# Performance work log

Measured on AMD Instinct MI355X. Metric: run time of the kernel, lower is better.

Reference implementation:

```python
import jax, jax.numpy as jnp
import numpy as np
import math

PHI = (1 + math.sqrt(5)) / 2
ALPHA = 1 / PHI          # residual scale
BETA = 1 / PHI ** 2      # sparse-matmul scale
DIM = 1910
NZ = int(DIM * DIM / PHI)


def setup_inputs() -> dict:
    key = jax.random.key(0)
    kx, ki, kv = jax.random.split(key, 3)
    x = jax.random.normal(kx, (8, 4096, DIM), dtype=jnp.float32)
    W_indices = jax.random.randint(ki, (2, NZ), 0, DIM, dtype=jnp.int32)
    W_values = jax.random.normal(kv, (NZ,), dtype=jnp.float32) / math.sqrt(DIM)
    return {"x": x, "W_indices": W_indices, "W_values": W_values}


def reference(x, W_indices, W_values):
    dim = x.shape[-1]
    # COO -> dense: duplicate (row,col) entries sum, matching torch.sparse semantics.
    W = jnp.zeros((dim, dim), dtype=x.dtype).at[W_indices[0], W_indices[1]].add(W_values)
    orig_shape = x.shape
    xf = x.reshape(-1, dim)          # [tokens, dim]
    Wx = xf @ W.T                    # (W @ x.T).T == x @ W.T
    out = ALPHA * xf + BETA * Wx
    return out.reshape(orig_shape)
```

## Files before the change

kernel.cpp:

```cpp
#include <hip/hip_runtime.h>
#include <hip/hip_bf16.h>
#include <stdint.h>

#define DIMV 1910
#define KP   1920
#define NT   30
#define TT   120
#define PHI_F  1.6180339887498949f
#define BETA_F 0.3819660112501051f

typedef __attribute__((ext_vector_type(4))) float f32x4;
typedef __attribute__((ext_vector_type(8))) short bf16x8;
typedef __attribute__((ext_vector_type(8))) unsigned short u16x8;

__device__ __forceinline__ void gl16(const void* g, void* l) {
    __builtin_amdgcn_global_load_lds(
        (const __attribute__((address_space(1))) void*)(uintptr_t)g,
        (__attribute__((address_space(3))) void*)(uint32_t)(uintptr_t)l,
        16, 0, 0);
}

__global__ void k_prep(const float* __restrict__ x, unsigned short* __restrict__ xb, int total8,
                       const int* __restrict__ ridx, const int* __restrict__ cidx,
                       const float* __restrict__ vals, float* __restrict__ Wd, int nz) {
    const int tid  = threadIdx.x;
    const int half = (int)gridDim.x >> 1;
    const int b    = (int)blockIdx.x >> 1;
    const int stride = half * 256;
    if ((blockIdx.x & 1) == 0) {
        for (int i = b * 256 + tid; i < total8; i += stride) {
            int v = i * 8;
            int row = v / KP;
            int col = v - row * KP;
            u16x8 o;
            if (col + 8 <= DIMV) {
                const float2* s = (const float2*)(x + (size_t)row * DIMV + col);
                float2 f0 = s[0], f1 = s[1], f2 = s[2], f3 = s[3];
                float f[8] = {f0.x, f0.y, f1.x, f1.y, f2.x, f2.y, f3.x, f3.y};
#pragma unroll
                for (int j = 0; j < 8; ++j) {
                    __hip_bfloat16 bb = __float2bfloat16(f[j]);
                    o[j] = *reinterpret_cast<unsigned short*>(&bb);
                }
            } else {
#pragma unroll
                for (int j = 0; j < 8; ++j) {
                    int c = col + j;
                    float fv = (c < DIMV) ? x[(size_t)row * DIMV + c] : 0.f;
                    __hip_bfloat16 bb = __float2bfloat16(fv);
                    o[j] = *reinterpret_cast<unsigned short*>(&bb);
                }
            }
            *(u16x8*)(xb + (size_t)v) = o;
        }
    } else {
        for (int i = b * 256 + tid; i < nz; i += stride)
            atomicAdd(Wd + (size_t)ridx[i] * DIMV + cidx[i], vals[i]);
    }
}

__global__ void k_build_w(const float* __restrict__ Wd, unsigned short* __restrict__ Wb, int total8) {
    int stride = gridDim.x * blockDim.x;
    for (int i = blockIdx.x * blockDim.x + threadIdx.x; i < total8; i += stride) {
        int v = i * 8;
        int n = v / KP;
        int k = v - n * KP;
        u16x8 o;
#pragma unroll
        for (int j = 0; j < 8; ++j) {
            int kk = k + j;
            float fv = (n < DIMV && kk < DIMV) ? Wd[(size_t)n * DIMV + kk] : 0.f;
            if (kk == n && n < DIMV) fv += PHI_F;
            __hip_bfloat16 b = __float2bfloat16(fv);
            o[j] = *reinterpret_cast<unsigned short*>(&b);
        }
        *(u16x8*)(Wb + (size_t)v) = o;
    }
}

__global__ __launch_bounds__(512, 2) void k_gemm(const short* __restrict__ A,
                                                 const short* __restrict__ B,
                                                 float* __restrict__ C) {
    __shared__ char lds[163840];

    const int bid = blockIdx.x;
    const int bmg = bid & 31;
    const int bn  = bid >> 5;

    const int tid = threadIdx.x;
    const int w   = tid >> 6;
    const int l   = tid & 63;
    const int wm  = w >> 2;
    const int wn  = w & 3;
    const int fr  = l & 15;
    const int q   = l >> 4;

    const int    srow = tid >> 3;
    const size_t KPB  = (size_t)KP * 2;
    const int    swz  = ((tid & 7) ^ (srow & 7)) * 16;
    const char*  bSrc = (const char*)B + (size_t)(bn * 256 + srow) * KPB + swz;
    const size_t sweep = (size_t)64 * KPB;
    char* stDst = lds + tid * 16;

    const int co0  = ((q    ) ^ (fr & 7)) * 16;
    const int co1  = ((4 + q) ^ (fr & 7)) * 16;
    const int aOff = (wm * 128 + fr) * 128;
    const int bOff = (wn * 64 + fr) * 128;

    f32x4 acc[8][4] = {};

#define STAGE_A(src, kk_, dstoff, s) gl16((src) + (size_t)(s) * sweep + (size_t)(kk_) * 128, stDst + (dstoff) + (s) * 8192)
#define STAGE_B(kk_, dstoff, s)      gl16(bSrc  + (size_t)(s) * sweep + (size_t)(kk_) * 128, stDst + 98304 + (dstoff) + (s) * 8192)

    const char* aSrc0 = (const char*)A + (size_t)(bmg * 256 + srow) * KPB + swz;
    const size_t mstep = (size_t)8192 * KPB;

#pragma unroll
    for (int s = 0; s < 4; ++s) STAGE_A(aSrc0, 0, 0, s);
#pragma unroll
    for (int s = 0; s < 4; ++s) STAGE_B(0, 0, s);
#pragma unroll
    for (int s = 0; s < 4; ++s) STAGE_A(aSrc0, 1, 32768, s);
    asm volatile("s_waitcnt vmcnt(4)" ::: "memory");
    __builtin_amdgcn_s_barrier();
    asm volatile("" ::: "memory");

    int boA = 0, stA = 65536;
    int boB = 0, stB = 32768;
    int tkR = 0;
    int kb1 = 1;
    int ka2 = 2;
    int mtR = 0;
    const char* aStage = aSrc0;

    for (int t = 0; t < TT; ++t) {
        const char* pa = lds + boA + aOff;
        const char* pb = lds + 98304 + boB + bOff;
        const bool stb = (t + 1 < TT);
        const bool sta = (t + 2 < TT);
        bf16x8 a[4][2], b0[2][2], b1[2][2];

#pragma unroll
        for (int mi = 0; mi < 4; ++mi) {
            a[mi][0] = *(const bf16x8*)(pa + mi * 2048 + co0);
            a[mi][1] = *(const bf16x8*)(pa + mi * 2048 + co1);
        }
#pragma unroll
        for (int ni = 0; ni < 2; ++ni) {
            b0[ni][0] = *(const bf16x8*)(pb + ni * 2048 + co0);
            b0[ni][1] = *(const bf16x8*)(pb + ni * 2048 + co1);
        }
        if (stb) { STAGE_B(kb1, stB, 0); STAGE_B(kb1, stB, 1); }
        asm volatile("s_waitcnt lgkmcnt(8)" ::: "memory");
        __builtin_amdgcn_s_barrier();
        asm volatile("s_waitcnt lgkmcnt(0)" ::: "memory");
        __builtin_amdgcn_sched_barrier(0);
        __builtin_amdgcn_s_setprio(1);
#pragma unroll
        for (int kk = 0; kk < 2; ++kk)
#pragma unroll
            for (int mi = 0; mi < 4; ++mi)
#pragma unroll
                for (int ni = 0; ni < 2; ++ni)
                    acc[mi][ni] = __builtin_amdgcn_mfma_f32_16x16x32_bf16(a[mi][kk], b0[ni][kk], acc[mi][ni], 0, 0, 0);
        __builtin_amdgcn_s_setprio(0);
        asm volatile("" ::: "memory");
        __builtin_amdgcn_s_barrier();
        asm volatile("" ::: "memory");

#pragma unroll
        for (int ni = 0; ni < 2; ++ni) {
            b1[ni][0] = *(const bf16x8*)(pb + 4096 + ni * 2048 + co0);
            b1[ni][1] = *(const bf16x8*)(pb + 4096 + ni * 2048 + co1);
        }
        if (stb) { STAGE_B(kb1, stB, 2); STAGE_B(kb1, stB, 3); }
        if (sta) { STAGE_A(aStage, ka2, stA, 0); STAGE_A(aStage, ka2, stA, 1); }
        asm volatile("" ::: "memory");
        __builtin_amdgcn_s_barrier();
        asm volatile("s_waitcnt lgkmcnt(0)" ::: "memory");
        __builtin_amdgcn_sched_barrier(0);
        __builtin_amdgcn_s_setprio(1);
#pragma unroll
        for (int kk = 0; kk < 2; ++kk)
#pragma unroll
            for (int mi = 0; mi < 4; ++mi)
#pragma unroll
                for (int ni = 0; ni < 2; ++ni)
                    acc[mi][ni + 2] = __builtin_amdgcn_mfma_f32_16x16x32_bf16(a[mi][kk], b1[ni][kk], acc[mi][ni + 2], 0, 0, 0);
        __builtin_amdgcn_s_setprio(0);
        asm volatile("" ::: "memory");
        __builtin_amdgcn_s_barrier();
        asm volatile("" ::: "memory");

#pragma unroll
        for (int mi = 0; mi < 4; ++mi) {
            a[mi][0] = *(const bf16x8*)(pa + 8192 + mi * 2048 + co0);
            a[mi][1] = *(const bf16x8*)(pa + 8192 + mi * 2048 + co1);
        }
        if (sta) { STAGE_A(aStage, ka2, stA, 2); STAGE_A(aStage, ka2, stA, 3); }
        asm volatile("" ::: "memory");
        __builtin_amdgcn_s_barrier();
        asm volatile("s_waitcnt lgkmcnt(0)" ::: "memory");
        __builtin_amdgcn_sched_barrier(0);
        __builtin_amdgcn_s_setprio(1);
#pragma unroll
        for (int kk = 0; kk < 2; ++kk)
#pragma unroll
            for (int mi = 0; mi < 4; ++mi)
#pragma unroll
                for (int ni = 0; ni < 2; ++ni)
                    acc[mi + 4][ni + 2] = __builtin_amdgcn_mfma_f32_16x16x32_bf16(a[mi][kk], b1[ni][kk], acc[mi + 4][ni + 2], 0, 0, 0);
#pragma unroll
        for (int kk = 0; kk < 2; ++kk)
#pragma unroll
            for (int mi = 0; mi < 4; ++mi)
#pragma unroll
                for (int ni = 0; ni < 2; ++ni)
                    acc[mi + 4][ni] = __builtin_amdgcn_mfma_f32_16x16x32_bf16(a[mi][kk], b0[ni][kk], acc[mi + 4][ni], 0, 0, 0);
        __builtin_amdgcn_s_setprio(0);
        if (sta) { asm volatile("s_waitcnt vmcnt(4)" ::: "memory"); }
        else     { asm volatile("s_waitcnt vmcnt(0)" ::: "memory"); }
        __builtin_amdgcn_s_barrier();
        asm volatile("" ::: "memory");

        if (tkR == NT - 1) {
            const int bm    = mtR * 32 + bmg;
            const int grow0 = bm * 256 + wm * 128 + q * 4;
            const int gcol0 = bn * 256 + wn * 64 + fr;
#pragma unroll
            for (int ei = 0; ei < 8; ++ei) {
#pragma unroll
                for (int ni = 0; ni < 4; ++ni) {
                    int gcol = gcol0 + ni * 16;
                    if (gcol < DIMV) {
                        size_t base = (size_t)(grow0 + ei * 16) * DIMV + gcol;
#pragma unroll
                        for (int r = 0; r < 4; ++r)
                            C[base + (size_t)r * DIMV] = BETA_F * acc[ei][ni][r];
                    }
                }
            }
            if (t + 1 < TT) {
#pragma unroll
                for (int ei = 0; ei < 8; ++ei)
#pragma unroll
                    for (int ni = 0; ni < 4; ++ni)
                        acc[ei][ni] = (f32x4)(0.f);
            }
            tkR = 0; ++mtR;
        } else ++tkR;

        boA = (boA == 65536) ? 0 : boA + 32768;
        stA = (stA == 65536) ? 0 : stA + 32768;
        boB ^= 32768;
        stB ^= 32768;
        if (++kb1 == NT) kb1 = 0;
        if (++ka2 == NT) { ka2 = 0; aStage += mstep; }
    }
#undef STAGE_A
#undef STAGE_B
}

extern "C" void kernel_launch(void* const* d_in, const int* in_sizes, int n_in,
                              void* d_out, int out_size, void* d_ws, size_t ws_size,
                              hipStream_t stream) {
    const float* x    = (const float*)d_in[0];
    const int*   widx = (const int*)d_in[1];
    const float* wval = (const float*)d_in[2];
    float* out = (float*)d_out;

    const int nz = in_sizes[2];
    const int M  = in_sizes[0] / DIMV;

    const size_t xb_bytes = (size_t)M * KP * 2;
    const size_t wb_bytes = (size_t)2048 * KP * 2;
    const size_t wd_bytes = (size_t)DIMV * DIMV * 4;
    char* ws = (char*)d_ws;
    unsigned short* xb = (unsigned short*)ws;
    unsigned short* Wb = (unsigned short*)(ws + xb_bytes);
    float*          Wd = (float*)(ws + xb_bytes + wb_bytes);
    if (ws_size < xb_bytes + wb_bytes + wd_bytes) return;

    hipMemsetAsync(Wd, 0, wd_bytes, stream);
    k_prep<<<2048, 256, 0, stream>>>(x, xb, M * KP / 8, widx, widx + nz, wval, Wd, nz);
    k_build_w<<<1800, 256, 0, stream>>>(Wd, Wb, KP * KP / 8);
    k_gemm<<<256, 512, 0, stream>>>((const short*)xb, (const short*)Wb, out);
}
```

Before: 390.2 us.

## Restructure GEMM main loop into two-phase double-buffered LDS with register prefetch

Replaces the four-phase loop (triple-buffered A, double-buffered B) with a two-phase loop. A and B are both double-buffered in LDS, which shrinks the shared allocation to 128 KB. Each iteration loads the next k-slice's first fragments into registers while the current second-half MMAs run, and issues all global→LDS stages for iteration t+2 in one group. This halves the barriers per iteration and lengthens the MFMA runs, at the cost of more live operand registers and a full vmcnt(0) wait each iteration.

```diff
diff --git a/kernel.cpp b/kernel.cpp
--- a/kernel.cpp
+++ b/kernel.cpp
@@ -81,7 +81,7 @@
 __global__ __launch_bounds__(512, 2) void k_gemm(const short* __restrict__ A,
                                                  const short* __restrict__ B,
                                                  float* __restrict__ C) {
-    __shared__ char lds[163840];
+    __shared__ char lds[131072];
 
     const int bid = blockIdx.x;
     const int bmg = bid & 31;
@@ -108,9 +108,16 @@
     const int bOff = (wn * 64 + fr) * 128;
 
     f32x4 acc[8][4] = {};
-
-#define STAGE_A(src, kk_, dstoff, s) gl16((src) + (size_t)(s) * sweep + (size_t)(kk_) * 128, stDst + (dstoff) + (s) * 8192)
-#define STAGE_B(kk_, dstoff, s)      gl16(bSrc  + (size_t)(s) * sweep + (size_t)(kk_) * 128, stDst + 98304 + (dstoff) + (s) * 8192)
+    bf16x8 aP0[8], aP1[8], bR0[4], bR1[4];
+
+#define STAGE_A(src, kk_, slot, s) gl16((src) + (size_t)(s) * sweep + (size_t)(kk_) * 128, stDst + (slot) + (s) * 8192)
+#define STAGE_B(kk_, slot, s)      gl16(bSrc  + (size_t)(s) * sweep + (size_t)(kk_) * 128, stDst + 65536 + (slot) + (s) * 8192)
+#define MM(bank, bb)                                                             \
+    _Pragma("unroll")                                                            \
+    for (int mi = 0; mi < 8; ++mi)                                               \
+        _Pragma("unroll")                                                        \
+        for (int ni = 0; ni < 4; ++ni)                                           \
+            acc[mi][ni] = __builtin_amdgcn_mfma_f32_16x16x32_bf16((bank)[mi], (bb)[ni], acc[mi][ni], 0, 0, 0);
 
     const char* aSrc0 = (const char*)A + (size_t)(bmg * 256 + srow) * KPB + swz;
     const size_t mstep = (size_t)8192 * KPB;
@@ -121,107 +128,65 @@
     for (int s = 0; s < 4; ++s) STAGE_B(0, 0, s);
 #pragma unroll
     for (int s = 0; s < 4; ++s) STAGE_A(aSrc0, 1, 32768, s);
-    asm volatile("s_waitcnt vmcnt(4)" ::: "memory");
+#pragma unroll
+    for (int s = 0; s < 4; ++s) STAGE_B(1, 32768, s);
+    asm volatile("s_waitcnt vmcnt(8)" ::: "memory");
     __builtin_amdgcn_s_barrier();
-    asm volatile("" ::: "memory");
-
-    int boA = 0, stA = 65536;
-    int boB = 0, stB = 32768;
-    int tkR = 0;
-    int kb1 = 1;
-    int ka2 = 2;
-    int mtR = 0;
+    __builtin_amdgcn_sched_barrier(0);
+#pragma unroll
+    for (int mi = 0; mi < 8; ++mi) aP0[mi] = *(const bf16x8*)(lds + aOff + mi * 2048 + co0);
+#pragma unroll
+    for (int ni = 0; ni < 4; ++ni) bR0[ni] = *(const bf16x8*)(lds + 65536 + bOff + ni * 2048 + co0);
+
+    int bo  = 0;
+    int k2  = 2;
+    int tkR = 0, mtR = 0;
     const char* aStage = aSrc0;
 
     for (int t = 0; t < TT; ++t) {
-        const char* pa = lds + boA + aOff;
-        const char* pb = lds + 98304 + boB + bOff;
-        const bool stb = (t + 1 < TT);
-        const bool sta = (t + 2 < TT);
-        bf16x8 a[4][2], b0[2][2], b1[2][2];
-
-#pragma unroll
-        for (int mi = 0; mi < 4; ++mi) {
-            a[mi][0] = *(const bf16x8*)(pa + mi * 2048 + co0);
-            a[mi][1] = *(const bf16x8*)(pa + mi * 2048 + co1);
-        }
-#pragma unroll
-        for (int ni = 0; ni < 2; ++ni) {
-            b0[ni][0] = *(const bf16x8*)(pb + ni * 2048 + co0);
-            b0[ni][1] = *(const bf16x8*)(pb + ni * 2048 + co1);
-        }
-        if (stb) { STAGE_B(kb1, stB, 0); STAGE_B(kb1, stB, 1); }
-        asm volatile("s_waitcnt lgkmcnt(8)" ::: "memory");
+        const int nbo = bo ^ 32768;
+        const char* pa  = lds + bo + aOff;
+        const char* pb  = lds + 65536 + bo + bOff;
+        const char* paN = lds + nbo + aOff;
+        const char* pbN = lds + 65536 + nbo + bOff;
+        const bool haveN = (t + 1 < TT);
+        const bool have2 = (t + 2 < TT);
+
         __builtin_amdgcn_s_barrier();
+        __builtin_amdgcn_sched_barrier(0);
+#pragma unroll
+        for (int mi = 0; mi < 8; ++mi) aP1[mi] = *(const bf16x8*)(pa + mi * 2048 + co1);
+#pragma unroll
+        for (int ni = 0; ni < 4; ++ni) bR1[ni] = *(const bf16x8*)(pb + ni * 2048 + co1);
+        __builtin_amdgcn_sched_barrier(0);
+        __builtin_amdgcn_s_setprio(1);
+        MM(aP0, bR0)
+        __builtin_amdgcn_s_setprio(0);
+        asm volatile("s_waitcnt vmcnt(0)" ::: "memory");
         asm volatile("s_waitcnt lgkmcnt(0)" ::: "memory");
         __builtin_amdgcn_sched_barrier(0);
+
+        __builtin_amdgcn_s_barrier();
+        __builtin_amdgcn_sched_barrier(0);
+        if (haveN) {
+#pragma unroll
+            for (int mi = 0; mi < 8; ++mi) aP0[mi] = *(const bf16x8*)(paN + mi * 2048 + co0);
+#pragma unroll
+            for (int ni = 0; ni < 4; ++ni) bR0[ni] = *(const bf16x8*)(pbN + ni * 2048 + co0);
+        }
+        if (have2) {
+            STAGE_A(aStage, k2, bo, 0); STAGE_A(aStage, k2, bo, 1);
+            STAGE_A(aStage, k2, bo, 2); STAGE_A(aStage, k2, bo, 3);
+            STAGE_B(k2, bo, 0); STAGE_B(k2, bo, 1);
+            STAGE_B(k2, bo, 2); STAGE_B(k2, bo, 3);
+        }
+        __builtin_amdgcn_sched_barrier(0);
         __builtin_amdgcn_s_setprio(1);
-#pragma unroll
-        for (int kk = 0; kk < 2; ++kk)
-#pragma unroll
-            for (int mi = 0; mi < 4; ++mi)
-#pragma unroll
-                for (int ni = 0; ni < 2; ++ni)
-                    acc[mi][ni] = __builtin_amdgcn_mfma_f32_16x16x32_bf16(a[mi][kk], b0[ni][kk], acc[mi][ni], 0, 0, 0);
+        MM(aP1, bR1)
         __builtin_amdgcn_s_setprio(0);
-        asm volatile("" ::: "memory");
-        __builtin_amdgcn_s_barrier();
-        asm volatile("" ::: "memory");
-
-#pragma unroll
-        for (int ni = 0; ni < 2; ++ni) {
-            b1[ni][0] = *(const bf16x8*)(pb + 4096 + ni * 2048 + co0);
-            b1[ni][1] = *(const bf16x8*)(pb + 4096 + ni * 2048 + co1);
-        }
-        if (stb) { STAGE_B(kb1, stB, 2); STAGE_B(kb1, stB, 3); }
-        if (sta) { STAGE_A(aStage, ka2, stA, 0); STAGE_A(aStage, ka2, stA, 1); }
-        asm volatile("" ::: "memory");
-        __builtin_amdgcn_s_barrier();
+        asm volatile("s_waitcnt vmcnt(8)" ::: "memory");
         asm volatile("s_waitcnt lgkmcnt(0)" ::: "memory");
         __builtin_amdgcn_sched_barrier(0);
-        __builtin_amdgcn_s_setprio(1);
-#pragma unroll
-        for (int kk = 0; kk < 2; ++kk)
-#pragma unroll
-            for (int mi = 0; mi < 4; ++mi)
-#pragma unroll
-                for (int ni = 0; ni < 2; ++ni)
-                    acc[mi][ni + 2] = __builtin_amdgcn_mfma_f32_16x16x32_bf16(a[mi][kk], b1[ni][kk], acc[mi][ni + 2], 0, 0, 0);
-        __builtin_amdgcn_s_setprio(0);
-        asm volatile("" ::: "memory");
-        __builtin_amdgcn_s_barrier();
-        asm volatile("" ::: "memory");
-
-#pragma unroll
-        for (int mi = 0; mi < 4; ++mi) {
-            a[mi][0] = *(const bf16x8*)(pa + 8192 + mi * 2048 + co0);
-            a[mi][1] = *(const bf16x8*)(pa + 8192 + mi * 2048 + co1);
-        }
-        if (sta) { STAGE_A(aStage, ka2, stA, 2); STAGE_A(aStage, ka2, stA, 3); }
-        asm volatile("" ::: "memory");
-        __builtin_amdgcn_s_barrier();
-        asm volatile("s_waitcnt lgkmcnt(0)" ::: "memory");
-        __builtin_amdgcn_sched_barrier(0);
-        __builtin_amdgcn_s_setprio(1);
-#pragma unroll
-        for (int kk = 0; kk < 2; ++kk)
-#pragma unroll
-            for (int mi = 0; mi < 4; ++mi)
-#pragma unroll
-                for (int ni = 0; ni < 2; ++ni)
-                    acc[mi + 4][ni + 2] = __builtin_amdgcn_mfma_f32_16x16x32_bf16(a[mi][kk], b1[ni][kk], acc[mi + 4][ni + 2], 0, 0, 0);
-#pragma unroll
-        for (int kk = 0; kk < 2; ++kk)
-#pragma unroll
-            for (int mi = 0; mi < 4; ++mi)
-#pragma unroll
-                for (int ni = 0; ni < 2; ++ni)
-                    acc[mi + 4][ni] = __builtin_amdgcn_mfma_f32_16x16x32_bf16(a[mi][kk], b0[ni][kk], acc[mi + 4][ni], 0, 0, 0);
-        __builtin_amdgcn_s_setprio(0);
-        if (sta) { asm volatile("s_waitcnt vmcnt(4)" ::: "memory"); }
-        else     { asm volatile("s_waitcnt vmcnt(0)" ::: "memory"); }
-        __builtin_amdgcn_s_barrier();
-        asm volatile("" ::: "memory");
 
         if (tkR == NT - 1) {
             const int bm    = mtR * 32 + bmg;
@@ -240,7 +205,7 @@
                     }
                 }
             }
-            if (t + 1 < TT) {
+            if (haveN) {
 #pragma unroll
                 for (int ei = 0; ei < 8; ++ei)
 #pragma unroll
@@ -250,15 +215,12 @@
             tkR = 0; ++mtR;
         } else ++tkR;
 
-        boA = (boA == 65536) ? 0 : boA + 32768;
-        stA = (stA == 65536) ? 0 : stA + 32768;
-        boB ^= 32768;
-        stB ^= 32768;
-        if (++kb1 == NT) kb1 = 0;
-        if (++ka2 == NT) { ka2 = 0; aStage += mstep; }
+        bo = nbo;
+        if (++k2 == NT) { k2 = 0; aStage += mstep; }
     }
 #undef STAGE_A
 #undef STAGE_B
+#undef MM
 }
 
 extern "C" void kernel_launch(void* const* d_in, const int* in_sizes, int n_in,
```

Measured after the change: 404.4 us. +3.6%, slower.
